# Performance work log

Hardware: AMD Instinct MI355X
Metric: run time of the kernel (lower is better)

## Reference

```python
import jax, jax.numpy as jnp
import numpy as np

N = 100000
IN_C = 128
HID = 16
HEADS = 8
OUT_C = 64
E = 1600000
NEG_SLOPE = 0.2
EPS = 1e-16


def setup_inputs() -> dict:
    key = jax.random.key(0)
    ks = jax.random.split(key, 12)
    s = lambda k, shape, fan: jax.random.normal(k, shape, jnp.float32) * (1.0 / np.sqrt(fan))
    return {
        "x": jax.random.normal(ks[0], (N, IN_C), jnp.float32),
        "edge_index": jax.random.randint(ks[1], (2, E), 0, N, jnp.int64),
        # conv1 params (heads=8, concat=True)
        "W1": s(ks[2], (IN_C, HEADS * HID), IN_C),
        "a_src1": s(ks[3], (HEADS, HID), HID),
        "a_dst1": s(ks[4], (HEADS, HID), HID),
        "b1": jnp.zeros((HEADS * HID,), jnp.float32),
        # conv2 params (heads=1, concat=False)
        "W2": s(ks[5], (HEADS * HID, OUT_C), HEADS * HID),
        "a_src2": s(ks[6], (1, OUT_C), OUT_C),
        "a_dst2": s(ks[7], (1, OUT_C), OUT_C),
        "b2": jnp.zeros((OUT_C,), jnp.float32),
    }


def gat_conv(x, src, dst, W, a_src, a_dst, bias, concat):
    """PyG-style GATConv: edge softmax over incoming edges + scatter-add."""
    H, C = a_src.shape
    n = x.shape[0]
    h = (x @ W).reshape(n, H, C)                      # [N,H,C]
    asrc = jnp.einsum("nhc,hc->nh", h, a_src)          # [N,H]
    adst = jnp.einsum("nhc,hc->nh", h, a_dst)          # [N,H]
    e = jax.nn.leaky_relu(asrc[src] + adst[dst], NEG_SLOPE)  # [E,H]
    # numerically-stable segment softmax over edges sharing a destination
    m = jax.ops.segment_max(e, dst, num_segments=n)    # [N,H]
    m = jnp.where(jnp.isfinite(m), m, 0.0)
    ex = jnp.exp(e - m[dst])                           # [E,H]
    denom = jax.ops.segment_sum(ex, dst, num_segments=n)  # [N,H]
    alpha = ex / (denom[dst] + EPS)                    # [E,H]
    out = jax.ops.segment_sum(alpha[:, :, None] * h[src], dst, num_segments=n)  # [N,H,C]
    out = out.reshape(n, H * C) if concat else out.mean(axis=1)
    return out + bias


def reference(x, edge_index, W1, a_src1, a_dst1, b1, W2, a_src2, a_dst2, b2):
    n = x.shape[0]
    # PyG GATConv adds self-loops by default
    loop = jnp.arange(n, dtype=edge_index.dtype)
    src = jnp.concatenate([edge_index[0], loop])
    dst = jnp.concatenate([edge_index[1], loop])
    # dropout(p=0.6) is identity at inference
    h = jax.nn.elu(gat_conv(x, src, dst, W1, a_src1, a_dst1, b1, concat=True))
    return gat_conv(h, src, dst, W2, a_src2, a_dst2, b2, concat=False)
```

## Files before the change

kernel.cpp:

```cpp
#include <hip/hip_runtime.h>
#include <hip/hip_bf16.h>
#include <math.h>


typedef __attribute__((ext_vector_type(8))) short short8;
typedef __attribute__((ext_vector_type(4))) float f32x4;

__device__ __forceinline__ float bflo(uint u) { return __uint_as_float(u << 16); }
__device__ __forceinline__ float bfhi(uint u) { return __uint_as_float(u & 0xffff0000u); }
__device__ __forceinline__ float bfs(ushort v) { return __uint_as_float(((uint)v) << 16); }
__device__ __forceinline__ ushort f2bf(float f) {
    uint u = __float_as_uint(f);
    u += 0x7fff + ((u >> 16) & 1);
    return (ushort)(u >> 16);
}
#define LOG2E 1.44269504088896f

#define CSR_CAP 4096

__global__ __launch_bounds__(256) void k_bhist(const int* __restrict__ dst, int e,
                                               int* __restrict__ bcount) {
    __shared__ int h[1024];
    int t = threadIdx.x;
    for (int i = t; i < 1024; i += 256) h[i] = 0;
    __syncthreads();
    int c0 = blockIdx.x * 4096, c1 = min(c0 + 4096, e);
    for (int i = c0 + t; i < c1; i += 256) atomicAdd(&h[dst[i] >> 7], 1);
    __syncthreads();
    for (int i = t; i < 1024; i += 256)
        if (h[i]) atomicAdd(&bcount[i], h[i]);
}

__global__ __launch_bounds__(256) void k_bscan(const int* __restrict__ bcount, int nb, int n,
                                               int* __restrict__ ebase, int* __restrict__ ecur,
                                               int* __restrict__ cbase) {
    __shared__ int ae[1024], be[1024], ac[1024], bc[1024];
    int t = threadIdx.x;
    for (int i = t; i < 1024; i += 256) {
        int v = 0, nn = 0;
        if (i < nb) {
            v = bcount[i];
            nn = min(128, n - (i << 7));
        }
        ae[i] = v;
        ac[i] = v + nn;
    }
    __syncthreads();
    int* pa = ae; int* qa = be; int* pc = ac; int* qc = bc;
    for (int off = 1; off < 1024; off <<= 1) {
        for (int i = t; i < 1024; i += 256) {
            int va = pa[i], vc = pc[i];
            if (i >= off) { va += pa[i - off]; vc += pc[i - off]; }
            qa[i] = va; qc[i] = vc;
        }
        __syncthreads();
        int* tm = pa; pa = qa; qa = tm;
        tm = pc; pc = qc; qc = tm;
    }
    for (int i = t; i < 1024; i += 256) {
        if (i < nb) {
            int ea = (i == 0) ? 0 : pa[i - 1];
            int ca = (i == 0) ? 0 : pc[i - 1];
            ebase[i] = ea; ecur[i] = ea; cbase[i] = ca;
        }
    }
}

__global__ __launch_bounds__(256) void k_part(const int* __restrict__ src,
                                              const int* __restrict__ dst, int e,
                                              int* __restrict__ ecur, int* __restrict__ ebuf) {
    __shared__ int h[1024];
    __shared__ int base[1024];
    int t = threadIdx.x;
    int c0 = blockIdx.x * 4096, c1 = min(c0 + 4096, e);
    for (int i = t; i < 1024; i += 256) h[i] = 0;
    __syncthreads();
    for (int i = c0 + t; i < c1; i += 256) atomicAdd(&h[dst[i] >> 7], 1);
    __syncthreads();
    for (int i = t; i < 1024; i += 256) {
        int c = h[i];
        base[i] = c ? atomicAdd(&ecur[i], c) : 0;
        h[i] = 0;
    }
    __syncthreads();
    for (int i = c0 + t; i < c1; i += 256) {
        int d = dst[i], b = d >> 7;
        int r = atomicAdd(&h[b], 1);
        ebuf[base[b] + r] = (src[i] << 7) | (d & 127);
    }
}

__global__ __launch_bounds__(256) void k_build(const int* __restrict__ ebuf,
                                               const int* __restrict__ bcount,
                                               const int* __restrict__ ebase,
                                               const int* __restrict__ cbase,
                                               int* __restrict__ rowptr,
                                               int* __restrict__ csr,
                                               int* __restrict__ dstid, int n, int nb) {
    __shared__ int cnt[128];
    __shared__ int sc[128], sc2[128];
    __shared__ int csr_l[CSR_CAP];
    __shared__ int dst_l[CSR_CAP];
    int b = blockIdx.x, t = threadIdx.x;
    int n0 = b << 7;
    int nn = min(128, n - n0);
    int ec = bcount[b], eb = ebase[b], cb = cbase[b];
    if (t < 128) cnt[t] = 0;
    __syncthreads();
    for (int i = t; i < ec; i += 256) atomicAdd(&cnt[ebuf[eb + i] & 127], 1);
    __syncthreads();
    if (t < 128) sc[t] = (t < nn) ? cnt[t] + 1 : 0;
    __syncthreads();
    int* p = sc; int* q = sc2;
    for (int off = 1; off < 128; off <<= 1) {
        if (t < 128) {
            int v = p[t];
            if (t >= off) v += p[t - off];
            q[t] = v;
        }
        __syncthreads();
        int* tm = p; p = q; q = tm;
    }
    int total = p[127];
    if (total <= CSR_CAP) {
        if (t < nn) {
            int off = (t == 0) ? 0 : p[t - 1];
            rowptr[n0 + t] = cb + off;
            csr_l[off] = n0 + t;
            dst_l[off] = n0 + t;
            cnt[t] = off + 1;
        }
        __syncthreads();
        for (int i = t; i < ec; i += 256) {
            int v = ebuf[eb + i];
            int d = v & 127;
            int s = atomicAdd(&cnt[d], 1);
            csr_l[s] = v >> 7;
            dst_l[s] = n0 + d;
        }
        __syncthreads();
        for (int i = t; i < total; i += 256) {
            csr[cb + i] = csr_l[i];
            dstid[cb + i] = dst_l[i];
        }
    } else {
        if (t < nn) {
            int off = (t == 0) ? 0 : p[t - 1];
            rowptr[n0 + t] = cb + off;
            csr[cb + off] = n0 + t;
            dstid[cb + off] = n0 + t;
            cnt[t] = off + 1;
        }
        __syncthreads();
        for (int i = t; i < ec; i += 256) {
            int v = ebuf[eb + i];
            int d = v & 127;
            int s = atomicAdd(&cnt[d], 1);
            csr[cb + s] = v >> 7;
            dstid[cb + s] = n0 + d;
        }
    }
    if (b == nb - 1 && t == 0) rowptr[n] = cb + total;
}

template <int COLS, bool XBF16>
__global__ __launch_bounds__(256) void k_gemm_mfma(const void* __restrict__ Xv,
                                                   const float* __restrict__ W,
                                                   ushort* __restrict__ Y, int n) {
    __shared__ ushort As[128][136];
    __shared__ ushort Ws[COLS][136];
    const int t = threadIdx.x;
    const int row0 = blockIdx.x * 128;
    if constexpr (!XBF16) {
        const float* X = (const float*)Xv;
#pragma unroll
        for (int q = 0; q < 16; q++) {
            int idx = t + q * 256;
            int r = idx >> 5, c4 = (idx & 31) * 4;
            float4 xv = make_float4(0.f, 0.f, 0.f, 0.f);
            if (row0 + r < n) xv = *reinterpret_cast<const float4*>(&X[(size_t)(row0 + r) * 128 + c4]);
            ushort4 w4 = make_ushort4(f2bf(xv.x), f2bf(xv.y), f2bf(xv.z), f2bf(xv.w));
            *reinterpret_cast<ushort4*>(&As[r][c4]) = w4;
        }
    } else {
        const ushort* X = (const ushort*)Xv;
#pragma unroll
        for (int q = 0; q < 8; q++) {
            int idx = t + q * 256;
            int r = idx >> 4, c8 = (idx & 15) * 8;
            uint4 v = make_uint4(0u, 0u, 0u, 0u);
            if (row0 + r < n) v = *reinterpret_cast<const uint4*>(&X[(size_t)(row0 + r) * 128 + c8]);
            *reinterpret_cast<uint4*>(&As[r][c8]) = v;
        }
    }
    for (int i = t; i < 128 * COLS; i += 256) {
        int k = i / COLS, nc = i % COLS;
        Ws[nc][k] = f2bf(W[i]);
    }
    __syncthreads();
    const int w = t >> 6, l = t & 63;
    const int lr = l & 15;
    const int lk = (l >> 4) * 8;
    f32x4 acc[2][COLS / 16];
#pragma unroll
    for (int m = 0; m < 2; m++)
#pragma unroll
        for (int nb = 0; nb < COLS / 16; nb++) acc[m][nb] = (f32x4){0.f, 0.f, 0.f, 0.f};
#pragma unroll
    for (int kc = 0; kc < 128; kc += 32) {
        short8 a0 = *reinterpret_cast<const short8*>(&As[w * 32 + lr][kc + lk]);
        short8 a1 = *reinterpret_cast<const short8*>(&As[w * 32 + 16 + lr][kc + lk]);
#pragma unroll
        for (int nb = 0; nb < COLS / 16; nb++) {
            short8 bf = *reinterpret_cast<const short8*>(&Ws[nb * 16 + lr][kc + lk]);
            acc[0][nb] = __builtin_amdgcn_mfma_f32_16x16x32_bf16(a0, bf, acc[0][nb], 0, 0, 0);
            acc[1][nb] = __builtin_amdgcn_mfma_f32_16x16x32_bf16(a1, bf, acc[1][nb], 0, 0, 0);
        }
    }
#pragma unroll
    for (int m = 0; m < 2; m++)
#pragma unroll
        for (int j = 0; j < 4; j++) {
            int r = row0 + w * 32 + m * 16 + (l >> 4) * 4 + j;
            if (r < n) {
#pragma unroll
                for (int nb = 0; nb < COLS / 16; nb++)
                    Y[(size_t)r * COLS + nb * 16 + lr] = f2bf(acc[m][nb][j]);
            }
        }
}

__global__ void k_attn1(const uint* __restrict__ hu, const float* __restrict__ a_src,
                        const float* __restrict__ a_dst, float* __restrict__ asrc,
                        float* __restrict__ adst, int n) {
    int t = blockIdx.x * 256 + threadIdx.x;
    if (t >= n * 8) return;
    int node = t >> 3, hd = t & 7;
    const uint* hp = hu + (size_t)node * 64 + hd * 8;
    float s1 = 0.f, s2 = 0.f;
#pragma unroll
    for (int q = 0; q < 8; q++) {
        uint u = hp[q];
        float v0 = bflo(u), v1 = bfhi(u);
        s1 = fmaf(v0, a_src[hd * 16 + 2 * q], s1);
        s1 = fmaf(v1, a_src[hd * 16 + 2 * q + 1], s1);
        s2 = fmaf(v0, a_dst[hd * 16 + 2 * q], s2);
        s2 = fmaf(v1, a_dst[hd * 16 + 2 * q + 1], s2);
    }
    asrc[t] = s1 * LOG2E;
    adst[t] = s2 * LOG2E;
}
__global__ void k_attn2(const uint* __restrict__ hu, const float* __restrict__ a_src,
                        const float* __restrict__ a_dst, float* __restrict__ asrc,
                        float* __restrict__ adst, int n) {
    int t = blockIdx.x * 256 + threadIdx.x;
    if (t >= n * 8) return;
    int node = t >> 3, j = t & 7;
    const uint* hp = hu + (size_t)node * 32 + j * 4;
    float s1 = 0.f, s2 = 0.f;
#pragma unroll
    for (int q = 0; q < 4; q++) {
        uint u = hp[q];
        float v0 = bflo(u), v1 = bfhi(u);
        s1 = fmaf(v0, a_src[j * 8 + 2 * q], s1);
        s1 = fmaf(v1, a_src[j * 8 + 2 * q + 1], s1);
        s2 = fmaf(v0, a_dst[j * 8 + 2 * q], s2);
        s2 = fmaf(v1, a_dst[j * 8 + 2 * q + 1], s2);
    }
#pragma unroll
    for (int o = 1; o < 8; o <<= 1) {
        s1 += __shfl_xor(s1, o);
        s2 += __shfl_xor(s2, o);
    }
    if (j == 0) { asrc[node] = s1 * LOG2E; adst[node] = s2 * LOG2E; }
}

__global__ void k_score1(const int* __restrict__ csr, const int* __restrict__ dstid,
                         const float* __restrict__ asrc, const float* __restrict__ adst,
                         _Float16* __restrict__ p1, int tot8) {
    int t = blockIdx.x * 256 + threadIdx.x;
    if (t >= tot8) return;
    int slot = t >> 3, hd = t & 7;
    int s = csr[slot], d = dstid[slot];
    float e = asrc[s * 8 + hd] + adst[d * 8 + hd];
    e = fmaxf(e, 0.2f * e);
    p1[t] = (_Float16)exp2f(e);
}
__global__ void k_score2(const int* __restrict__ csr, const int* __restrict__ dstid,
                         const float* __restrict__ asrc, const float* __restrict__ adst,
                         float* __restrict__ p2, int tot) {
    int t = blockIdx.x * 256 + threadIdx.x;
    if (t >= tot) return;
    float e = asrc[csr[t]] + adst[dstid[t]];
    e = fmaxf(e, 0.2f * e);
    p2[t] = exp2f(e);
}

__global__ __launch_bounds__(256) void k_agg1(
    const uint* __restrict__ hu, const _Float16* __restrict__ p1,
    const int* __restrict__ rowptr, const int* __restrict__ csr,
    const float* __restrict__ b1, uint* __restrict__ x2, int n) {
    int wid = (blockIdx.x * 256 + threadIdx.x) >> 6;
    if (wid >= n) return;
    uint lane = threadIdx.x & 63;
    uint c0 = lane * 2;
    uint hd = lane >> 3;
    int beg = rowptr[wid], end = rowptr[wid + 1];
    float s = 0.f, acc0 = 0.f, acc1 = 0.f;
    for (int base = beg; base < end; base += 64) {
        int cnt = min(64, end - base);
        int vidx = ((int)lane < cnt) ? csr[base + lane] : 0;
        const _Float16* pp = p1 + (size_t)base * 8 + hd;
        int j = 0;
        for (; j + 4 <= cnt; j += 4) {
            uint s0 = __builtin_amdgcn_readlane(vidx, j);
            uint s1 = __builtin_amdgcn_readlane(vidx, j + 1);
            uint s2 = __builtin_amdgcn_readlane(vidx, j + 2);
            uint s3 = __builtin_amdgcn_readlane(vidx, j + 3);
            float q0 = (float)pp[(j + 0) * 8];
            float q1 = (float)pp[(j + 1) * 8];
            float q2 = (float)pp[(j + 2) * 8];
            float q3 = (float)pp[(j + 3) * 8];
            uint u0 = hu[s0 * 64u + lane];
            uint u1 = hu[s1 * 64u + lane];
            uint u2 = hu[s2 * 64u + lane];
            uint u3 = hu[s3 * 64u + lane];
            s += (q0 + q1) + (q2 + q3);
            acc0 = fmaf(q0, bflo(u0), fmaf(q1, bflo(u1), acc0));
            acc0 = fmaf(q2, bflo(u2), fmaf(q3, bflo(u3), acc0));
            acc1 = fmaf(q0, bfhi(u0), fmaf(q1, bfhi(u1), acc1));
            acc1 = fmaf(q2, bfhi(u2), fmaf(q3, bfhi(u3), acc1));
        }
        for (; j < cnt; ++j) {
            uint s0 = __builtin_amdgcn_readlane(vidx, j);
            float q0 = (float)pp[j * 8];
            uint u0 = hu[s0 * 64u + lane];
            s += q0;
            acc0 = fmaf(q0, bflo(u0), acc0);
            acc1 = fmaf(q0, bfhi(u0), acc1);
        }
    }
    float inv = 1.f / (s + 1e-16f);
    float o0 = acc0 * inv + b1[c0];
    float o1 = acc1 * inv + b1[c0 + 1];
    o0 = o0 > 0.f ? o0 : (__expf(o0) - 1.f);
    o1 = o1 > 0.f ? o1 : (__expf(o1) - 1.f);
    union { ushort b[2]; uint u; } pk;
    pk.b[0] = f2bf(o0);
    pk.b[1] = f2bf(o1);
    x2[(uint)wid * 64u + lane] = pk.u;
}
__global__ __launch_bounds__(256) void k_agg2(
    const ushort* __restrict__ hb, const float* __restrict__ p2,
    const int* __restrict__ rowptr, const int* __restrict__ csr,
    const float* __restrict__ b2, float* __restrict__ out, int n) {
    int wid = (blockIdx.x * 256 + threadIdx.x) >> 6;
    if (wid >= n) return;
    uint lane = threadIdx.x & 63;
    int beg = rowptr[wid], end = rowptr[wid + 1];
    float s = 0.f, acc = 0.f;
    for (int base = beg; base < end; base += 64) {
        int cnt = min(64, end - base);
        int vidx = ((int)lane < cnt) ? csr[base + lane] : 0;
        int pvi = ((int)lane < cnt) ? __float_as_int(p2[base + lane]) : 0;
        int j = 0;
        for (; j + 4 <= cnt; j += 4) {
            uint s0 = __builtin_amdgcn_readlane(vidx, j);
            uint s1 = __builtin_amdgcn_readlane(vidx, j + 1);
            uint s2 = __builtin_amdgcn_readlane(vidx, j + 2);
            uint s3 = __builtin_amdgcn_readlane(vidx, j + 3);
            float q0 = __int_as_float(__builtin_amdgcn_readlane(pvi, j));
            float q1 = __int_as_float(__builtin_amdgcn_readlane(pvi, j + 1));
            float q2 = __int_as_float(__builtin_amdgcn_readlane(pvi, j + 2));
            float q3 = __int_as_float(__builtin_amdgcn_readlane(pvi, j + 3));
            float h0 = bfs(hb[s0 * 64u + lane]);
            float h1 = bfs(hb[s1 * 64u + lane]);
            float h2 = bfs(hb[s2 * 64u + lane]);
            float h3 = bfs(hb[s3 * 64u + lane]);
            s += (q0 + q1) + (q2 + q3);
            acc = fmaf(q0, h0, fmaf(q1, h1, acc));
            acc = fmaf(q2, h2, fmaf(q3, h3, acc));
        }
        for (; j < cnt; ++j) {
            uint s0 = __builtin_amdgcn_readlane(vidx, j);
            float q0 = __int_as_float(__builtin_amdgcn_readlane(pvi, j));
            float h0 = bfs(hb[s0 * 64u + lane]);
            s += q0;
            acc = fmaf(q0, h0, acc);
        }
    }
    out[(size_t)wid * 64 + lane] = acc / (s + 1e-16f) + b2[lane];
}

extern "C" void kernel_launch(void* const* d_in, const int* in_sizes, int n_in,
                              void* d_out, int out_size, void* d_ws, size_t ws_size,
                              hipStream_t stream) {
    const float* x   = (const float*)d_in[0];
    const int*   ei  = (const int*)d_in[1];
    const float* W1  = (const float*)d_in[2];
    const float* as1 = (const float*)d_in[3];
    const float* ad1 = (const float*)d_in[4];
    const float* b1  = (const float*)d_in[5];
    const float* W2  = (const float*)d_in[6];
    const float* as2 = (const float*)d_in[7];
    const float* ad2 = (const float*)d_in[8];
    const float* b2  = (const float*)d_in[9];
    float* out = (float*)d_out;

    int N = in_sizes[0] / 128;
    int E = in_sizes[1] / 2;
    int TOT = E + N;
    const int* src = ei;
    const int* dst = ei + E;

    char* p = (char*)d_ws;
    auto alloc = [&](size_t bytes) {
        char* r = p;
        p += (bytes + 255) & ~size_t(255);
        return r;
    };
    ushort* h1b  = (ushort*)alloc((size_t)N * 128 * 2);
    ushort* h2b  = (ushort*)alloc((size_t)N * 64 * 2);
    ushort* x2b  = (ushort*)alloc((size_t)N * 128 * 2);
    float* asrc1 = (float*)alloc((size_t)N * 8 * 4);
    float* adst1 = (float*)alloc((size_t)N * 8 * 4);
    float* asrc2 = (float*)alloc((size_t)N * 4);
    float* adst2 = (float*)alloc((size_t)N * 4);
    int* rowptr  = (int*)alloc((size_t)(N + 1) * 4);
    int* csr     = (int*)alloc((size_t)TOT * 4);
    int* dstid   = (int*)alloc((size_t)TOT * 4);
    int* ebuf    = (int*)alloc((size_t)TOT * 4);
    _Float16* p1 = (_Float16*)alloc((size_t)TOT * 8 * 2);
    int* bcount  = (int*)alloc(1024 * 4);
    int* ebase   = (int*)alloc(1024 * 4);
    int* ecur    = (int*)alloc(1024 * 4);
    int* cbase   = (int*)alloc(1024 * 4);
    float* p2    = (float*)ebuf;

    int NB = (N + 127) >> 7;
    int nbk = (E + 4095) / 4096;

    hipMemsetAsync(bcount, 0, 1024 * 4, stream);
    k_bhist<<<nbk, 256, 0, stream>>>(dst, E, bcount);
    k_bscan<<<1, 256, 0, stream>>>(bcount, NB, N, ebase, ecur, cbase);
    k_part<<<nbk, 256, 0, stream>>>(src, dst, E, ecur, ebuf);
    k_build<<<NB, 256, 0, stream>>>(ebuf, bcount, ebase, cbase, rowptr, csr, dstid, N, NB);

    int gb = (N + 127) / 128;
    k_gemm_mfma<128, false><<<gb, 256, 0, stream>>>(x, W1, h1b, N);
    k_attn1<<<(N * 8 + 255) / 256, 256, 0, stream>>>((const uint*)h1b, as1, ad1, asrc1, adst1, N);
    k_score1<<<((size_t)TOT * 8 + 255) / 256, 256, 0, stream>>>(csr, dstid, asrc1, adst1, p1, TOT * 8);
    k_agg1<<<(N + 3) / 4, 256, 0, stream>>>((const uint*)h1b, p1, rowptr, csr, b1, (uint*)x2b, N);

    k_gemm_mfma<64, true><<<gb, 256, 0, stream>>>(x2b, W2, h2b, N);
    k_attn2<<<(N * 8 + 255) / 256, 256, 0, stream>>>((const uint*)h2b, as2, ad2, asrc2, adst2, N);
    k_score2<<<(TOT + 255) / 256, 256, 0, stream>>>(csr, dstid, asrc2, adst2, p2, TOT);
    k_agg2<<<(N + 3) / 4, 256, 0, stream>>>((const ushort*)h2b, p2, rowptr, csr, b2, out, N);
}
```

Measured before the change: 275.9 us.

## Fuse edge score computation into aggregation kernels and drop dstid array

```diff
diff --git a/kernel.cpp b/kernel.cpp
--- a/kernel.cpp
+++ b/kernel.cpp
@@ -8,7 +8,6 @@
 
 __device__ __forceinline__ float bflo(uint u) { return __uint_as_float(u << 16); }
 __device__ __forceinline__ float bfhi(uint u) { return __uint_as_float(u & 0xffff0000u); }
-__device__ __forceinline__ float bfs(ushort v) { return __uint_as_float(((uint)v) << 16); }
 __device__ __forceinline__ ushort f2bf(float f) {
     uint u = __float_as_uint(f);
     u += 0x7fff + ((u >> 16) & 1);
@@ -95,12 +94,10 @@
                                                const int* __restrict__ ebase,
                                                const int* __restrict__ cbase,
                                                int* __restrict__ rowptr,
-                                               int* __restrict__ csr,
-                                               int* __restrict__ dstid, int n, int nb) {
+                                               int* __restrict__ csr, int n, int nb) {
     __shared__ int cnt[128];
     __shared__ int sc[128], sc2[128];
     __shared__ int csr_l[CSR_CAP];
-    __shared__ int dst_l[CSR_CAP];
     int b = blockIdx.x, t = threadIdx.x;
     int n0 = b << 7;
     int nn = min(128, n - n0);
@@ -127,37 +124,28 @@
             int off = (t == 0) ? 0 : p[t - 1];
             rowptr[n0 + t] = cb + off;
             csr_l[off] = n0 + t;
-            dst_l[off] = n0 + t;
             cnt[t] = off + 1;
         }
         __syncthreads();
         for (int i = t; i < ec; i += 256) {
             int v = ebuf[eb + i];
-            int d = v & 127;
-            int s = atomicAdd(&cnt[d], 1);
+            int s = atomicAdd(&cnt[v & 127], 1);
             csr_l[s] = v >> 7;
-            dst_l[s] = n0 + d;
         }
         __syncthreads();
-        for (int i = t; i < total; i += 256) {
-            csr[cb + i] = csr_l[i];
-            dstid[cb + i] = dst_l[i];
-        }
+        for (int i = t; i < total; i += 256) csr[cb + i] = csr_l[i];
     } else {
         if (t < nn) {
             int off = (t == 0) ? 0 : p[t - 1];
             rowptr[n0 + t] = cb + off;
             csr[cb + off] = n0 + t;
-            dstid[cb + off] = n0 + t;
             cnt[t] = off + 1;
         }
         __syncthreads();
         for (int i = t; i < ec; i += 256) {
             int v = ebuf[eb + i];
-            int d = v & 127;
-            int s = atomicAdd(&cnt[d], 1);
+            int s = atomicAdd(&cnt[v & 127], 1);
             csr[cb + s] = v >> 7;
-            dstid[cb + s] = n0 + d;
         }
     }
     if (b == nb - 1 && t == 0) rowptr[n] = cb + total;
@@ -275,121 +263,113 @@
     if (j == 0) { asrc[node] = s1 * LOG2E; adst[node] = s2 * LOG2E; }
 }
 
-__global__ void k_score1(const int* __restrict__ csr, const int* __restrict__ dstid,
-                         const float* __restrict__ asrc, const float* __restrict__ adst,
-                         _Float16* __restrict__ p1, int tot8) {
-    int t = blockIdx.x * 256 + threadIdx.x;
-    if (t >= tot8) return;
-    int slot = t >> 3, hd = t & 7;
-    int s = csr[slot], d = dstid[slot];
-    float e = asrc[s * 8 + hd] + adst[d * 8 + hd];
-    e = fmaxf(e, 0.2f * e);
-    p1[t] = (_Float16)exp2f(e);
-}
-__global__ void k_score2(const int* __restrict__ csr, const int* __restrict__ dstid,
-                         const float* __restrict__ asrc, const float* __restrict__ adst,
-                         float* __restrict__ p2, int tot) {
-    int t = blockIdx.x * 256 + threadIdx.x;
-    if (t >= tot) return;
-    float e = asrc[csr[t]] + adst[dstid[t]];
-    e = fmaxf(e, 0.2f * e);
-    p2[t] = exp2f(e);
-}
-
 __global__ __launch_bounds__(256) void k_agg1(
-    const uint* __restrict__ hu, const _Float16* __restrict__ p1,
-    const int* __restrict__ rowptr, const int* __restrict__ csr,
-    const float* __restrict__ b1, uint* __restrict__ x2, int n) {
+    const uint* __restrict__ hu, const float* __restrict__ asrc,
+    const float* __restrict__ adst, const int* __restrict__ rowptr,
+    const int* __restrict__ csr, const float* __restrict__ b1,
+    uint2* __restrict__ x2, int n) {
     int wid = (blockIdx.x * 256 + threadIdx.x) >> 6;
     if (wid >= n) return;
-    uint lane = threadIdx.x & 63;
-    uint c0 = lane * 2;
-    uint hd = lane >> 3;
+    int lane = threadIdx.x & 63;
+    int half = lane >> 5, cl = lane & 31;
+    int hd = cl >> 2;
+    int hsel = lane >> 3;
+    float adnm = adst[wid * 8 + hsel];
     int beg = rowptr[wid], end = rowptr[wid + 1];
-    float s = 0.f, acc0 = 0.f, acc1 = 0.f;
+    float s = 0.f, a0 = 0.f, a1 = 0.f, a2 = 0.f, a3 = 0.f;
     for (int base = beg; base < end; base += 64) {
         int cnt = min(64, end - base);
-        int vidx = ((int)lane < cnt) ? csr[base + lane] : 0;
-        const _Float16* pp = p1 + (size_t)base * 8 + hd;
-        int j = 0;
-        for (; j + 4 <= cnt; j += 4) {
-            uint s0 = __builtin_amdgcn_readlane(vidx, j);
-            uint s1 = __builtin_amdgcn_readlane(vidx, j + 1);
-            uint s2 = __builtin_amdgcn_readlane(vidx, j + 2);
-            uint s3 = __builtin_amdgcn_readlane(vidx, j + 3);
-            float q0 = (float)pp[(j + 0) * 8];
-            float q1 = (float)pp[(j + 1) * 8];
-            float q2 = (float)pp[(j + 2) * 8];
-            float q3 = (float)pp[(j + 3) * 8];
-            uint u0 = hu[s0 * 64u + lane];
-            uint u1 = hu[s1 * 64u + lane];
-            uint u2 = hu[s2 * 64u + lane];
-            uint u3 = hu[s3 * 64u + lane];
-            s += (q0 + q1) + (q2 + q3);
-            acc0 = fmaf(q0, bflo(u0), fmaf(q1, bflo(u1), acc0));
-            acc0 = fmaf(q2, bflo(u2), fmaf(q3, bflo(u3), acc0));
-            acc1 = fmaf(q0, bfhi(u0), fmaf(q1, bfhi(u1), acc1));
-            acc1 = fmaf(q2, bfhi(u2), fmaf(q3, bfhi(u3), acc1));
-        }
-        for (; j < cnt; ++j) {
-            uint s0 = __builtin_amdgcn_readlane(vidx, j);
-            float q0 = (float)pp[j * 8];
-            uint u0 = hu[s0 * 64u + lane];
-            s += q0;
-            acc0 = fmaf(q0, bflo(u0), acc0);
-            acc1 = fmaf(q0, bfhi(u0), acc1);
-        }
-    }
-    float inv = 1.f / (s + 1e-16f);
-    float o0 = acc0 * inv + b1[c0];
-    float o1 = acc1 * inv + b1[c0 + 1];
-    o0 = o0 > 0.f ? o0 : (__expf(o0) - 1.f);
-    o1 = o1 > 0.f ? o1 : (__expf(o1) - 1.f);
-    union { ushort b[2]; uint u; } pk;
-    pk.b[0] = f2bf(o0);
-    pk.b[1] = f2bf(o1);
-    x2[(uint)wid * 64u + lane] = pk.u;
+        int vidx = csr[base + min(lane, cnt - 1)];
+#pragma unroll
+        for (int k = 0; k < 8; k++) {
+            if (k * 8 < cnt) {
+                int sP = __shfl(vidx, k * 8 + (lane & 7));
+                float e = asrc[sP * 8 + hsel] + adnm;
+                e = fmaxf(e, 0.2f * e);
+                float Pk = exp2f(e);
+#pragma unroll
+                for (int j2 = 0; j2 < 4; j2++) {
+                    int e2 = k * 8 + 2 * j2;
+                    if (e2 < cnt) {
+                        int ee = e2 + half;
+                        int eec = min(ee, cnt - 1);
+                        float pe = __shfl(Pk, (eec & 7) | (hd << 3));
+                        int se = __shfl(vidx, eec);
+                        pe = (ee < cnt) ? pe : 0.f;
+                        uint2 u = *reinterpret_cast<const uint2*>(&hu[(uint)se * 64u + 2u * cl]);
+                        s += pe;
+                        a0 = fmaf(pe, bflo(u.x), a0);
+                        a1 = fmaf(pe, bfhi(u.x), a1);
+                        a2 = fmaf(pe, bflo(u.y), a2);
+                        a3 = fmaf(pe, bfhi(u.y), a3);
+                    }
+                }
+            }
+        }
+    }
+    s  += __shfl_xor(s, 32);
+    a0 += __shfl_xor(a0, 32);
+    a1 += __shfl_xor(a1, 32);
+    a2 += __shfl_xor(a2, 32);
+    a3 += __shfl_xor(a3, 32);
+    if (half == 0) {
+        float inv = 1.f / (s + 1e-16f);
+        float o0 = a0 * inv + b1[4 * cl + 0];
+        float o1 = a1 * inv + b1[4 * cl + 1];
+        float o2 = a2 * inv + b1[4 * cl + 2];
+        float o3 = a3 * inv + b1[4 * cl + 3];
+        o0 = o0 > 0.f ? o0 : (__expf(o0) - 1.f);
+        o1 = o1 > 0.f ? o1 : (__expf(o1) - 1.f);
+        o2 = o2 > 0.f ? o2 : (__expf(o2) - 1.f);
+        o3 = o3 > 0.f ? o3 : (__expf(o3) - 1.f);
+        uint2 pk;
+        pk.x = (uint)f2bf(o0) | ((uint)f2bf(o1) << 16);
+        pk.y = (uint)f2bf(o2) | ((uint)f2bf(o3) << 16);
+        x2[(uint)wid * 32u + cl] = pk;
+    }
 }
 __global__ __launch_bounds__(256) void k_agg2(
-    const ushort* __restrict__ hb, const float* __restrict__ p2,
-    const int* __restrict__ rowptr, const int* __restrict__ csr,
-    const float* __restrict__ b2, float* __restrict__ out, int n) {
+    const uint* __restrict__ hb, const float* __restrict__ asrc,
+    const float* __restrict__ adst, const int* __restrict__ rowptr,
+    const int* __restrict__ csr, const float* __restrict__ b2,
+    float2* __restrict__ out, int n) {
     int wid = (blockIdx.x * 256 + threadIdx.x) >> 6;
     if (wid >= n) return;
-    uint lane = threadIdx.x & 63;
+    int lane = threadIdx.x & 63;
+    int half = lane >> 5, cl = lane & 31;
+    float adn = adst[wid];
     int beg = rowptr[wid], end = rowptr[wid + 1];
-    float s = 0.f, acc = 0.f;
+    float s = 0.f, a0 = 0.f, a1 = 0.f;
     for (int base = beg; base < end; base += 64) {
         int cnt = min(64, end - base);
-        int vidx = ((int)lane < cnt) ? csr[base + lane] : 0;
-        int pvi = ((int)lane < cnt) ? __float_as_int(p2[base + lane]) : 0;
-        int j = 0;
-        for (; j + 4 <= cnt; j += 4) {
-            uint s0 = __builtin_amdgcn_readlane(vidx, j);
-            uint s1 = __builtin_amdgcn_readlane(vidx, j + 1);
-            uint s2 = __builtin_amdgcn_readlane(vidx, j + 2);
-            uint s3 = __builtin_amdgcn_readlane(vidx, j + 3);
-            float q0 = __int_as_float(__builtin_amdgcn_readlane(pvi, j));
-            float q1 = __int_as_float(__builtin_amdgcn_readlane(pvi, j + 1));
-            float q2 = __int_as_float(__builtin_amdgcn_readlane(pvi, j + 2));
-            float q3 = __int_as_float(__builtin_amdgcn_readlane(pvi, j + 3));
-            float h0 = bfs(hb[s0 * 64u + lane]);
-            float h1 = bfs(hb[s1 * 64u + lane]);
-            float h2 = bfs(hb[s2 * 64u + lane]);
-            float h3 = bfs(hb[s3 * 64u + lane]);
-            s += (q0 + q1) + (q2 + q3);
-            acc = fmaf(q0, h0, fmaf(q1, h1, acc));
-            acc = fmaf(q2, h2, fmaf(q3, h3, acc));
-        }
-        for (; j < cnt; ++j) {
-            uint s0 = __builtin_amdgcn_readlane(vidx, j);
-            float q0 = __int_as_float(__builtin_amdgcn_readlane(pvi, j));
-            float h0 = bfs(hb[s0 * 64u + lane]);
-            s += q0;
-            acc = fmaf(q0, h0, acc);
-        }
-    }
-    out[(size_t)wid * 64 + lane] = acc / (s + 1e-16f) + b2[lane];
+        int vidx = csr[base + min(lane, cnt - 1)];
+        float e = asrc[vidx] + adn;
+        e = fmaxf(e, 0.2f * e);
+        float pl = exp2f(e);
+#pragma unroll
+        for (int jj = 0; jj < 32; jj++) {
+            int e2 = 2 * jj;
+            if (e2 < cnt) {
+                int ee = e2 + half;
+                int eec = min(ee, cnt - 1);
+                float pe = __shfl(pl, eec);
+                int se = __shfl(vidx, eec);
+                pe = (ee < cnt) ? pe : 0.f;
+                uint u = hb[(uint)se * 32u + cl];
+                s += pe;
+                a0 = fmaf(pe, bflo(u), a0);
+                a1 = fmaf(pe, bfhi(u), a1);
+            }
+        }
+    }
+    s  += __shfl_xor(s, 32);
+    a0 += __shfl_xor(a0, 32);
+    a1 += __shfl_xor(a1, 32);
+    if (half == 0) {
+        float inv = 1.f / (s + 1e-16f);
+        out[(uint)wid * 32u + cl] = make_float2(a0 * inv + b2[2 * cl],
+                                                a1 * inv + b2[2 * cl + 1]);
+    }
 }
 
 extern "C" void kernel_launch(void* const* d_in, const int* in_sizes, int n_in,
@@ -428,14 +408,11 @@
     float* adst2 = (float*)alloc((size_t)N * 4);
     int* rowptr  = (int*)alloc((size_t)(N + 1) * 4);
     int* csr     = (int*)alloc((size_t)TOT * 4);
-    int* dstid   = (int*)alloc((size_t)TOT * 4);
-    int* ebuf    = (int*)alloc((size_t)TOT * 4);
-    _Float16* p1 = (_Float16*)alloc((size_t)TOT * 8 * 2);
+    int* ebuf    = (int*)alloc((size_t)E * 4);
     int* bcount  = (int*)alloc(1024 * 4);
     int* ebase   = (int*)alloc(1024 * 4);
     int* ecur    = (int*)alloc(1024 * 4);
     int* cbase   = (int*)alloc(1024 * 4);
-    float* p2    = (float*)ebuf;
 
     int NB = (N + 127) >> 7;
     int nbk = (E + 4095) / 4096;
@@ -444,16 +421,16 @@
     k_bhist<<<nbk, 256, 0, stream>>>(dst, E, bcount);
     k_bscan<<<1, 256, 0, stream>>>(bcount, NB, N, ebase, ecur, cbase);
     k_part<<<nbk, 256, 0, stream>>>(src, dst, E, ecur, ebuf);
-    k_build<<<NB, 256, 0, stream>>>(ebuf, bcount, ebase, cbase, rowptr, csr, dstid, N, NB);
+    k_build<<<NB, 256, 0, stream>>>(ebuf, bcount, ebase, cbase, rowptr, csr, N, NB);
 
     int gb = (N + 127) / 128;
     k_gemm_mfma<128, false><<<gb, 256, 0, stream>>>(x, W1, h1b, N);
     k_attn1<<<(N * 8 + 255) / 256, 256, 0, stream>>>((const uint*)h1b, as1, ad1, asrc1, adst1, N);
-    k_score1<<<((size_t)TOT * 8 + 255) / 256, 256, 0, stream>>>(csr, dstid, asrc1, adst1, p1, TOT * 8);
-    k_agg1<<<(N + 3) / 4, 256, 0, stream>>>((const uint*)h1b, p1, rowptr, csr, b1, (uint*)x2b, N);
+    k_agg1<<<(N + 3) / 4, 256, 0, stream>>>((const uint*)h1b, asrc1, adst1, rowptr, csr, b1,
+                                            (uint2*)x2b, N);
 
     k_gemm_mfma<64, true><<<gb, 256, 0, stream>>>(x2b, W2, h2b, N);
     k_attn2<<<(N * 8 + 255) / 256, 256, 0, stream>>>((const uint*)h2b, as2, ad2, asrc2, adst2, N);
-    k_score2<<<(TOT + 255) / 256, 256, 0, stream>>>(csr, dstid, asrc2, adst2, p2, TOT);
-    k_agg2<<<(N + 3) / 4, 256, 0, stream>>>((const ushort*)h2b, p2, rowptr, csr, b2, out, N);
-}
+    k_agg2<<<(N + 3) / 4, 256, 0, stream>>>((const uint*)h2b, asrc2, adst2, rowptr, csr, b2,
+                                            (float2*)out, N);
+}
```

Result: slower. 310.5 us (+12.6%).
